# Kernel optimization log

Hardware: AMD Instinct MI355X
Metric: run time of the kernel (lower is better)

## Reference

```python
import jax, jax.numpy as jnp
import numpy as np

N, R, IN_DIM, OUT_DIM, MODE = 16, 128, 64, 64, 16


def setup_inputs() -> dict:
    key = jax.random.key(0)
    k1, k2, k3, k4, k5 = jax.random.split(key, 5)
    # xavier_normal-like scale used by the torch init:
    # std = gain * sqrt(2/(fan_in+fan_out)) with gain = sqrt(in+out)/(in*out)
    fan = IN_DIM * OUT_DIM * MODE * MODE  # torch fans over last-dim slices; scale is tiny either way
    w_std = (1.0 / (IN_DIM * OUT_DIM)) * np.sqrt(IN_DIM + OUT_DIM)
    return {
        "X": jax.random.normal(k1, (N, R, R, IN_DIM), dtype=jnp.float32),
        "w_res": jax.random.normal(k2, (IN_DIM, OUT_DIM), dtype=jnp.float32) / np.sqrt(IN_DIM),
        "b_res": jax.random.normal(k3, (OUT_DIM,), dtype=jnp.float32) * 0.01,
        "fw0": jax.random.normal(k4, (IN_DIM, OUT_DIM, MODE, MODE, 2), dtype=jnp.float32) * w_std,
        "fw1": jax.random.normal(k5, (IN_DIM, OUT_DIM, MODE, MODE, 2), dtype=jnp.float32) * w_std,
    }


def reference(X, w_res, b_res, fw0, fw1):
    # X: [N, r, r, in_dim]
    n, r, _, _ = X.shape
    m = MODE
    res = X @ w_res + b_res                          # [N, r, r, out]
    Xp = jnp.transpose(X, (0, 3, 1, 2))              # [N, in, r, r]
    X_ft = jnp.fft.rfft2(Xp, s=(r, r), norm="ortho")  # [N, in, r, r//2+1] complex
    W0 = fw0[..., 0] + 1j * fw0[..., 1]              # [in, out, m, m] complex
    W1 = fw1[..., 0] + 1j * fw1[..., 1]
    top = jnp.einsum("nihw,iohw->nohw", X_ft[:, :, :m, :m], W0)
    bot = jnp.einsum("nihw,iohw->nohw", X_ft[:, :, -m:, :m], W1)
    Out_ft = jnp.zeros((n, OUT_DIM, r, r // 2 + 1), dtype=top.dtype)
    Out_ft = Out_ft.at[:, :, :m, :m].set(top)
    Out_ft = Out_ft.at[:, :, -m:, :m].set(bot)
    Y = jnp.fft.irfft2(Out_ft, s=(r, r), norm="ortho")  # [N, out, r, r]
    Y = jnp.transpose(Y, (0, 2, 3, 1))                   # [N, r, r, out]
    return jax.nn.silu(Y + res)
```

## Files before the change

### kernel.cpp

```cpp
#include <hip/hip_runtime.h>

#define NBATCH 16
#define RSZ 128
#define ICH 64
#define OCH 64
#define MODES 16
#define TMODES 32
#define PI2F 6.283185307179586f

typedef float f32x4 __attribute__((ext_vector_type(4)));
typedef short bf16x8 __attribute__((ext_vector_type(8)));
typedef unsigned short u16x8 __attribute__((ext_vector_type(8)));

static __device__ __forceinline__ ushort f2bf(float f) {
  union { float f; unsigned u; } v;
  v.f = f;
  unsigned r = v.u + 0x7FFFu + ((v.u >> 16) & 1u);
  return (ushort)(r >> 16);
}
static __device__ __forceinline__ float b2f(ushort u) {
  union { unsigned u; float f; } v;
  v.u = ((unsigned)u) << 16;
  return v.f;
}
static __device__ __forceinline__ float2 twid(int p) {
  float a = PI2F * (float)p * (1.0f / 128.0f);
  return make_float2(__cosf(a), __sinf(a));
}

#define TAB_EF 4096
#define TAB_WR 8192
#define TAB_T1 12288
#define TAB_E2 28672

#define PREP_BLOCKS 138
#define DFTX_BLOCKS 2048

__global__ __launch_bounds__(256) void k_main(const float* __restrict__ X,
                                              const float* __restrict__ fw0,
                                              const float* __restrict__ fw1,
                                              const float* __restrict__ w_res,
                                              ushort2* __restrict__ A2,
                                              ushort* __restrict__ fwT,
                                              ushort* __restrict__ tabs) {
  const int tid = threadIdx.x;
  if (blockIdx.x < PREP_BLOCKS) {
    const int b = blockIdx.x;
    if (b < 128) {
      const int tensor = b >> 6, i = b & 63;
      const float* fw = tensor ? fw1 : fw0;
      const int o = tid & 63, q = tid >> 6;
      const float* src = fw + ((size_t)(i * 64 + o) * 256 + q * 64) * 2;
      ushort2* dst = (ushort2*)fwT;
#pragma unroll 4
      for (int r2 = 0; r2 < 32; ++r2) {
        float4 v = *(const float4*)(src + r2 * 4);
        int r = r2 * 2;
        int mh0 = q * 4 + (r >> 4), w0 = r & 15;
        int mh1 = q * 4 + ((r + 1) >> 4), w1 = (r + 1) & 15;
        int t0 = tensor * 16 + mh0, t1 = tensor * 16 + mh1;
        ushort2 p0, p1;
        p0.x = f2bf(v.x); p0.y = f2bf(v.y);
        p1.x = f2bf(v.z); p1.y = f2bf(v.w);
        dst[(((size_t)w0 * 32 + t0) * 64 + i) * 64 + o] = p0;
        dst[(((size_t)w1 * 32 + t1) * 64 + i) * 64 + o] = p1;
      }
      return;
    }
    __shared__ float2 utp[128];
    if (tid < 128) utp[tid] = twid(tid);
    __syncthreads();
    const int pb = b - 128;
    if (pb == 0) {
      for (int e = tid; e < 4096; e += 256) {
        int x = e >> 5, mm = e & 31, w = mm >> 1, c = mm & 1;
        float2 u = utp[(w * x) & 127];
        tabs[TAB_EF + e] = f2bf(c ? -u.y : u.x);
      }
    } else if (pb == 1) {
      for (int e = tid; e < 4096; e += 256) {
        int o = e >> 6, i = e & 63;
        tabs[TAB_WR + e] = f2bf(w_res[i * 64 + o]);
      }
    } else if (pb < 6) {
      for (int k = tid; k < 4096; k += 256) {
        int e = (pb - 2) * 4096 + k;
        int m = e >> 8, kk = e & 255;
        int y = kk & 127, pl = kk >> 7;
        int t = m & 31, imr = m >> 5;
        int h = (t < 16) ? t : (t + 96);
        float2 u = utp[(h * y) & 127];
        float val = (!imr) ? (pl ? u.y : u.x) : (pl ? u.x : -u.y);
        tabs[TAB_T1 + e] = f2bf(val);
      }
    } else {
      for (int k = tid; k < 4096; k += 256) {
        int e = (pb - 6) * 4096 + k;
        int m = e >> 6, kk = e & 63;
        int y = m & 127, imr = m >> 7;
        int t = kk & 31, pl = kk >> 5;
        int h = (t < 16) ? t : (t + 96);
        float2 u = utp[(h * y) & 127];
        float val = (!imr) ? (pl ? -u.y : u.x) : (pl ? u.x : u.y);
        tabs[TAB_E2 + e] = f2bf(val);
      }
    }
    return;
  }
  __shared__ float2 ut[128];
  __shared__ ushort Tm[32][136];
  __shared__ ushort XT[64][136];
  const int row = blockIdx.x - PREP_BLOCKS;
  const float* Xr = X + (size_t)row * RSZ * ICH;
  float4 rv[8];
#pragma unroll
  for (int e = 0; e < 2; ++e) {
    int r = tid + e * 256;
    int i0 = (r & 15) * 4, x0 = (r >> 4) * 4;
    rv[e * 4 + 0] = *(const float4*)&Xr[(x0 + 0) * ICH + i0];
    rv[e * 4 + 1] = *(const float4*)&Xr[(x0 + 1) * ICH + i0];
    rv[e * 4 + 2] = *(const float4*)&Xr[(x0 + 2) * ICH + i0];
    rv[e * 4 + 3] = *(const float4*)&Xr[(x0 + 3) * ICH + i0];
  }
  if (tid < 128) ut[tid] = twid(tid);
  __syncthreads();
#pragma unroll
  for (int e = 0; e < 16; ++e) {
    int idx = tid + e * 256;
    int m = idx >> 7, x = idx & 127;
    int w = m >> 1, c = m & 1;
    float2 u = ut[(w * x) & 127];
    Tm[m][x] = f2bf(c ? -u.y : u.x);
  }
#pragma unroll
  for (int e = 0; e < 2; ++e) {
    int r = tid + e * 256;
    int i0 = (r & 15) * 4, x0 = (r >> 4) * 4;
#pragma unroll
    for (int p = 0; p < 4; ++p) {
      int i = i0 + p;
      int col = x0 ^ ((((i) >> 2) & 7) << 3);
      ushort4 pk;
      pk.x = f2bf(((const float*)&rv[e * 4 + 0])[p]);
      pk.y = f2bf(((const float*)&rv[e * 4 + 1])[p]);
      pk.z = f2bf(((const float*)&rv[e * 4 + 2])[p]);
      pk.w = f2bf(((const float*)&rv[e * 4 + 3])[p]);
      *(ushort4*)&XT[i][col] = pk;
    }
  }
  __syncthreads();
  const int wid = tid >> 6, lane = tid & 63;
  const int lr = lane & 15, lk = lane >> 4;
  f32x4 acc[2];
  acc[0] = (f32x4)(0.f);
  acc[1] = (f32x4)(0.f);
#pragma unroll
  for (int kt = 0; kt < 4; ++kt) {
    int kb = kt * 32 + lk * 8;
    bf16x8 a0 = *(const bf16x8*)&Tm[lr][kb];
    bf16x8 a1 = *(const bf16x8*)&Tm[16 + lr][kb];
    int i = wid * 16 + lr;
    int col = kb ^ (((i >> 2) & 7) << 3);
    bf16x8 b = *(const bf16x8*)&XT[i][col];
    acc[0] = __builtin_amdgcn_mfma_f32_16x16x32_bf16(a0, b, acc[0], 0, 0, 0);
    acc[1] = __builtin_amdgcn_mfma_f32_16x16x32_bf16(a1, b, acc[1], 0, 0, 0);
  }
  {
    const int i = wid * 16 + lr;
#pragma unroll
    for (int mt = 0; mt < 2; ++mt) {
      int wb = mt * 8 + lk * 2;
      ushort2 p0, p1;
      p0.x = f2bf(acc[mt][0]); p0.y = f2bf(acc[mt][1]);
      p1.x = f2bf(acc[mt][2]); p1.y = f2bf(acc[mt][3]);
      A2[((size_t)row * MODES + wb) * ICH + i] = p0;
      A2[((size_t)row * MODES + wb + 1) * ICH + i] = p1;
    }
  }
}

__global__ __launch_bounds__(512) void k_mid(const ushort2* __restrict__ A2,
                                             const ushort* __restrict__ tabs,
                                             const ushort* __restrict__ fwT,
                                             ushort* __restrict__ D) {
  const int n = blockIdx.x >> 4;
  const int w = blockIdx.x & 15;
  __shared__ ushort As[64][264];
  __shared__ float2 Bls[32][66];
  __shared__ ushort Cs[64][72];
  const int tid = threadIdx.x;
  {
    const int i0 = (tid & 15) * 4, y0 = (tid >> 4) * 4;
    u16x8 vy[4];
#pragma unroll
    for (int dy = 0; dy < 4; ++dy)
      vy[dy] = *(const u16x8*)&A2[((size_t)(n * RSZ + y0 + dy) * MODES + w) * ICH + i0];
#pragma unroll
    for (int p = 0; p < 4; ++p) {
      ushort4 re, im;
      re.x = vy[0][2 * p];     re.y = vy[1][2 * p];     re.z = vy[2][2 * p];     re.w = vy[3][2 * p];
      im.x = vy[0][2 * p + 1]; im.y = vy[1][2 * p + 1]; im.z = vy[2][2 * p + 1]; im.w = vy[3][2 * p + 1];
      *(ushort4*)&As[i0 + p][y0] = re;
      *(ushort4*)&As[i0 + p][128 + y0] = im;
    }
  }
  __syncthreads();
  const int wid = tid >> 6, lane = tid & 63;
  const int lr = lane & 15, lk = lane >> 4;
  {
    const int mt = wid >> 1, nh = wid & 1;
    f32x4 acc[2];
    acc[0] = (f32x4)(0.f);
    acc[1] = (f32x4)(0.f);
#pragma unroll
    for (int kt = 0; kt < 8; ++kt) {
      int kb = kt * 32 + lk * 8;
      bf16x8 a = *(const bf16x8*)&tabs[TAB_T1 + (mt * 16 + lr) * 256 + kb];
      bf16x8 b0 = *(const bf16x8*)&As[(nh * 2 + 0) * 16 + lr][kb];
      bf16x8 b1 = *(const bf16x8*)&As[(nh * 2 + 1) * 16 + lr][kb];
      acc[0] = __builtin_amdgcn_mfma_f32_16x16x32_bf16(a, b0, acc[0], 0, 0, 0);
      acc[1] = __builtin_amdgcn_mfma_f32_16x16x32_bf16(a, b1, acc[1], 0, 0, 0);
    }
#pragma unroll
    for (int nt2 = 0; nt2 < 2; ++nt2)
#pragma unroll
      for (int q = 0; q < 4; ++q) {
        int m = mt * 16 + lk * 4 + q;
        int t = m & 31, pl = m >> 5;
        int i = (nh * 2 + nt2) * 16 + lr;
        ((float*)&Bls[t][i])[pl] = acc[nt2][q];
      }
  }
  __syncthreads();
  const float sc = (w == 0) ? (1.f / 16384.f) : (2.f / 16384.f);
  float2 cacc[4];
  const ushort2* fwT2 = (const ushort2*)fwT;
#pragma unroll
  for (int p = 0; p < 4; ++p) {
    const int t = p * 8 + wid;
    const ushort2* Wcol = fwT2 + (size_t)(w * 32 + t) * 4096 + lane;
    float cr = 0.f, ci = 0.f;
#pragma unroll 8
    for (int i = 0; i < 64; ++i) {
      ushort2 wv = Wcol[i * 64];
      float wr = b2f(wv.x), wi = b2f(wv.y);
      float2 b = Bls[t][i];
      cr += b.x * wr - b.y * wi;
      ci += b.x * wi + b.y * wr;
    }
    cacc[p] = make_float2(cr * sc, ci * sc);
  }
  __syncthreads();
#pragma unroll
  for (int p = 0; p < 4; ++p) {
    const int t = p * 8 + wid;
    Cs[lane][t] = f2bf(cacc[p].x);
    Cs[lane][t + 32] = f2bf(cacc[p].y);
  }
  __syncthreads();
  f32x4 acc[2][4];
#pragma unroll
  for (int mi = 0; mi < 2; ++mi)
#pragma unroll
    for (int nt = 0; nt < 4; ++nt) acc[mi][nt] = (f32x4)(0.f);
#pragma unroll
  for (int kt = 0; kt < 2; ++kt) {
    int kb = kt * 32 + lk * 8;
    bf16x8 b[4];
#pragma unroll
    for (int nt = 0; nt < 4; ++nt) b[nt] = *(const bf16x8*)&Cs[nt * 16 + lr][kb];
#pragma unroll
    for (int mi = 0; mi < 2; ++mi) {
      bf16x8 a = *(const bf16x8*)&tabs[TAB_E2 + ((wid * 2 + mi) * 16 + lr) * 64 + kb];
#pragma unroll
      for (int nt = 0; nt < 4; ++nt)
        acc[mi][nt] = __builtin_amdgcn_mfma_f32_16x16x32_bf16(a, b[nt], acc[mi][nt], 0, 0, 0);
    }
  }
#pragma unroll
  for (int mi = 0; mi < 2; ++mi)
#pragma unroll
    for (int nt = 0; nt < 4; ++nt)
#pragma unroll
      for (int q = 0; q < 4; ++q) {
        int m = (wid * 2 + mi) * 16 + lk * 4 + q;
        int y = m & 127, pl = m >> 7;
        int o = nt * 16 + lr;
        D[((size_t)(n * RSZ + y) * MODES + w) * 128 + o * 2 + pl] = f2bf(acc[mi][nt][q]);
      }
}

__global__ __launch_bounds__(256) void k_final(const float* __restrict__ X,
                                               const ushort* __restrict__ D,
                                               const ushort* __restrict__ tabs,
                                               const float* __restrict__ b_res,
                                               float* __restrict__ out) {
  __shared__ ushort Ac[128][104];
  __shared__ ushort Bc[64][104];
  __shared__ float br[64];
  const int tid = threadIdx.x;
  const int row = blockIdx.x;
  const float* Xr = X + (size_t)row * RSZ * ICH;
#pragma unroll
  for (int j = 0; j < 8; ++j) {
    int k = tid + j * 256;
    int x = k >> 4, i0 = (k & 15) * 4;
    float4 v = *(const float4*)&Xr[x * ICH + i0];
    ushort4 pk;
    pk.x = f2bf(v.x); pk.y = f2bf(v.y); pk.z = f2bf(v.z); pk.w = f2bf(v.w);
    *(ushort4*)&Ac[x][i0] = pk;
  }
  {
    int x = tid >> 1, half = tid & 1;
    *(bf16x8*)&Ac[x][64 + half * 16] = *(const bf16x8*)&tabs[TAB_EF + x * 32 + half * 16];
    *(bf16x8*)&Ac[x][64 + half * 16 + 8] = *(const bf16x8*)&tabs[TAB_EF + x * 32 + half * 16 + 8];
  }
  {
    int o = tid >> 2, s = (tid & 3) * 16;
    *(bf16x8*)&Bc[o][s] = *(const bf16x8*)&tabs[TAB_WR + o * 64 + s];
    *(bf16x8*)&Bc[o][s + 8] = *(const bf16x8*)&tabs[TAB_WR + o * 64 + s + 8];
  }
#pragma unroll
  for (int j = 0; j < 4; ++j) {
    int idx = tid + j * 256;
    int w2 = idx >> 6, o = idx & 63;
    ushort2 v = *(const ushort2*)&D[(size_t)row * 2048 + w2 * 128 + o * 2];
    *(ushort2*)&Bc[o][64 + 2 * w2] = v;
  }
  if (tid < 64) br[tid] = b_res[tid];
  __syncthreads();
  const int wid = tid >> 6, lane = tid & 63;
  const int lr = lane & 15, lk = lane >> 4;
  f32x4 acc[2][4];
#pragma unroll
  for (int mi = 0; mi < 2; ++mi)
#pragma unroll
    for (int nt = 0; nt < 4; ++nt) acc[mi][nt] = (f32x4)(0.f);
#pragma unroll
  for (int kt = 0; kt < 3; ++kt) {
    int kb = kt * 32 + lk * 8;
    bf16x8 a0 = *(const bf16x8*)&Ac[(wid * 2 + 0) * 16 + lr][kb];
    bf16x8 a1 = *(const bf16x8*)&Ac[(wid * 2 + 1) * 16 + lr][kb];
    bf16x8 b[4];
#pragma unroll
    for (int nt = 0; nt < 4; ++nt) b[nt] = *(const bf16x8*)&Bc[nt * 16 + lr][kb];
#pragma unroll
    for (int nt = 0; nt < 4; ++nt) {
      acc[0][nt] = __builtin_amdgcn_mfma_f32_16x16x32_bf16(a0, b[nt], acc[0][nt], 0, 0, 0);
      acc[1][nt] = __builtin_amdgcn_mfma_f32_16x16x32_bf16(a1, b[nt], acc[1][nt], 0, 0, 0);
    }
  }
  float* orow = out + (size_t)row * RSZ * OCH;
#pragma unroll
  for (int mi = 0; mi < 2; ++mi)
#pragma unroll
    for (int nt = 0; nt < 4; ++nt)
#pragma unroll
      for (int q = 0; q < 4; ++q) {
        int x = (wid * 2 + mi) * 16 + lk * 4 + q;
        int o = nt * 16 + lr;
        float v = acc[mi][nt][q] + br[o];
        orow[x * OCH + o] = v / (1.f + __expf(-v));
      }
}

extern "C" void kernel_launch(void* const* d_in, const int* in_sizes, int n_in,
                              void* d_out, int out_size, void* d_ws, size_t ws_size,
                              hipStream_t stream) {
  (void)in_sizes; (void)n_in; (void)out_size; (void)ws_size;
  const float* X = (const float*)d_in[0];
  const float* w_res = (const float*)d_in[1];
  const float* b_res = (const float*)d_in[2];
  const float* fw0 = (const float*)d_in[3];
  const float* fw1 = (const float*)d_in[4];
  float* out = (float*)d_out;
  ushort* wsu = (ushort*)d_ws;
  ushort2* A2 = (ushort2*)wsu;
  ushort* Dbf = wsu + 4194304;
  ushort* fwT = Dbf + 4194304;
  ushort* tabs = fwT + 4194304;
  k_main<<<PREP_BLOCKS + DFTX_BLOCKS, 256, 0, stream>>>(X, fw0, fw1, w_res, A2, fwT, tabs);
  k_mid<<<NBATCH * MODES, 512, 0, stream>>>(A2, tabs, fwT, Dbf);
  k_final<<<NBATCH * RSZ, 256, 0, stream>>>(X, Dbf, tabs, b_res, out);
}
```

Baseline: 64.92 us.

## Compute residual projection in k_main and pass bf16 result to k_final

Moves the X@w_res residual GEMM into k_main, reusing the X tile already loaded and converted to bf16 there, and stores the result as bf16 in workspace. k_final then starts its accumulators from this residual and only runs the spectral K-chunk, so it no longer reads X in fp32 or the w_res table. This adds a bf16 residual write/read round trip, extra LDS in k_main, and rounds the residual to bf16 before the final add.

After: 67.42 us. 3.8% more time.

```diff
diff --git a/kernel.cpp b/kernel.cpp
--- a/kernel.cpp
+++ b/kernel.cpp
@@ -29,11 +29,10 @@
 }
 
 #define TAB_EF 4096
-#define TAB_WR 8192
 #define TAB_T1 12288
 #define TAB_E2 28672
 
-#define PREP_BLOCKS 138
+#define PREP_BLOCKS 137
 #define DFTX_BLOCKS 2048
 
 __global__ __launch_bounds__(256) void k_main(const float* __restrict__ X,
@@ -42,6 +41,7 @@
                                               const float* __restrict__ w_res,
                                               ushort2* __restrict__ A2,
                                               ushort* __restrict__ fwT,
+                                              ushort* __restrict__ resb,
                                               ushort* __restrict__ tabs) {
   const int tid = threadIdx.x;
   if (blockIdx.x < PREP_BLOCKS) {
@@ -77,14 +77,9 @@
         float2 u = utp[(w * x) & 127];
         tabs[TAB_EF + e] = f2bf(c ? -u.y : u.x);
       }
-    } else if (pb == 1) {
-      for (int e = tid; e < 4096; e += 256) {
-        int o = e >> 6, i = e & 63;
-        tabs[TAB_WR + e] = f2bf(w_res[i * 64 + o]);
-      }
-    } else if (pb < 6) {
+    } else if (pb < 5) {
       for (int k = tid; k < 4096; k += 256) {
-        int e = (pb - 2) * 4096 + k;
+        int e = (pb - 1) * 4096 + k;
         int m = e >> 8, kk = e & 255;
         int y = kk & 127, pl = kk >> 7;
         int t = m & 31, imr = m >> 5;
@@ -95,7 +90,7 @@
       }
     } else {
       for (int k = tid; k < 4096; k += 256) {
-        int e = (pb - 6) * 4096 + k;
+        int e = (pb - 5) * 4096 + k;
         int m = e >> 6, kk = e & 63;
         int y = m & 127, imr = m >> 7;
         int t = kk & 31, pl = kk >> 5;
@@ -110,6 +105,8 @@
   __shared__ float2 ut[128];
   __shared__ ushort Tm[32][136];
   __shared__ ushort XT[64][136];
+  __shared__ ushort Xrm[128][76];
+  __shared__ ushort wrTs[64][76];
   const int row = blockIdx.x - PREP_BLOCKS;
   const float* Xr = X + (size_t)row * RSZ * ICH;
   float4 rv[8];
@@ -122,6 +119,18 @@
     rv[e * 4 + 2] = *(const float4*)&Xr[(x0 + 2) * ICH + i0];
     rv[e * 4 + 3] = *(const float4*)&Xr[(x0 + 3) * ICH + i0];
   }
+  {
+    int i = tid >> 2, oq = (tid & 3) * 16;
+    float4 wv0 = *(const float4*)&w_res[i * 64 + oq + 0];
+    float4 wv1 = *(const float4*)&w_res[i * 64 + oq + 4];
+    float4 wv2 = *(const float4*)&w_res[i * 64 + oq + 8];
+    float4 wv3 = *(const float4*)&w_res[i * 64 + oq + 12];
+    const float* wr4[4] = {(const float*)&wv0, (const float*)&wv1, (const float*)&wv2, (const float*)&wv3};
+#pragma unroll
+    for (int k = 0; k < 4; ++k)
+#pragma unroll
+      for (int c = 0; c < 4; ++c) wrTs[oq + k * 4 + c][i] = f2bf(wr4[k][c]);
+  }
   if (tid < 128) ut[tid] = twid(tid);
   __syncthreads();
 #pragma unroll
@@ -136,16 +145,26 @@
   for (int e = 0; e < 2; ++e) {
     int r = tid + e * 256;
     int i0 = (r & 15) * 4, x0 = (r >> 4) * 4;
+    ushort cc[4][4];
+#pragma unroll
+    for (int xr = 0; xr < 4; ++xr) {
+      const float* rp = (const float*)&rv[e * 4 + xr];
+#pragma unroll
+      for (int p = 0; p < 4; ++p) cc[xr][p] = f2bf(rp[p]);
+    }
 #pragma unroll
     for (int p = 0; p < 4; ++p) {
       int i = i0 + p;
       int col = x0 ^ ((((i) >> 2) & 7) << 3);
       ushort4 pk;
-      pk.x = f2bf(((const float*)&rv[e * 4 + 0])[p]);
-      pk.y = f2bf(((const float*)&rv[e * 4 + 1])[p]);
-      pk.z = f2bf(((const float*)&rv[e * 4 + 2])[p]);
-      pk.w = f2bf(((const float*)&rv[e * 4 + 3])[p]);
+      pk.x = cc[0][p]; pk.y = cc[1][p]; pk.z = cc[2][p]; pk.w = cc[3][p];
       *(ushort4*)&XT[i][col] = pk;
+    }
+#pragma unroll
+    for (int xr = 0; xr < 4; ++xr) {
+      ushort4 pk;
+      pk.x = cc[xr][0]; pk.y = cc[xr][1]; pk.z = cc[xr][2]; pk.w = cc[xr][3];
+      *(ushort4*)&Xrm[x0 + xr][i0] = pk;
     }
   }
   __syncthreads();
@@ -175,6 +194,40 @@
       p1.x = f2bf(acc[mt][2]); p1.y = f2bf(acc[mt][3]);
       A2[((size_t)row * MODES + wb) * ICH + i] = p0;
       A2[((size_t)row * MODES + wb + 1) * ICH + i] = p1;
+    }
+  }
+  f32x4 acc2[2][4];
+#pragma unroll
+  for (int mi = 0; mi < 2; ++mi)
+#pragma unroll
+    for (int nt = 0; nt < 4; ++nt) acc2[mi][nt] = (f32x4)(0.f);
+#pragma unroll
+  for (int kt2 = 0; kt2 < 2; ++kt2) {
+    int kb = kt2 * 32 + lk * 8;
+    bf16x8 a[2];
+#pragma unroll
+    for (int mi = 0; mi < 2; ++mi) a[mi] = *(const bf16x8*)&Xrm[(wid * 2 + mi) * 16 + lr][kb];
+#pragma unroll
+    for (int nt = 0; nt < 4; ++nt) {
+      bf16x8 b = *(const bf16x8*)&wrTs[nt * 16 + lr][kb];
+#pragma unroll
+      for (int mi = 0; mi < 2; ++mi)
+        acc2[mi][nt] = __builtin_amdgcn_mfma_f32_16x16x32_bf16(a[mi], b, acc2[mi][nt], 0, 0, 0);
+    }
+  }
+  {
+    ushort* rp = resb + (size_t)row * 8192 + tid * 32;
+#pragma unroll
+    for (int mi = 0; mi < 2; ++mi) {
+      ushort4 c0, c1, c2, c3;
+      c0.x = f2bf(acc2[mi][0][0]); c0.y = f2bf(acc2[mi][0][1]); c0.z = f2bf(acc2[mi][0][2]); c0.w = f2bf(acc2[mi][0][3]);
+      c1.x = f2bf(acc2[mi][1][0]); c1.y = f2bf(acc2[mi][1][1]); c1.z = f2bf(acc2[mi][1][2]); c1.w = f2bf(acc2[mi][1][3]);
+      c2.x = f2bf(acc2[mi][2][0]); c2.y = f2bf(acc2[mi][2][1]); c2.z = f2bf(acc2[mi][2][2]); c2.w = f2bf(acc2[mi][2][3]);
+      c3.x = f2bf(acc2[mi][3][0]); c3.y = f2bf(acc2[mi][3][1]); c3.z = f2bf(acc2[mi][3][2]); c3.w = f2bf(acc2[mi][3][3]);
+      *(ushort4*)&rp[mi * 16 + 0] = c0;
+      *(ushort4*)&rp[mi * 16 + 4] = c1;
+      *(ushort4*)&rp[mi * 16 + 8] = c2;
+      *(ushort4*)&rp[mi * 16 + 12] = c3;
     }
   }
 }
@@ -290,44 +343,35 @@
       }
 }
 
-__global__ __launch_bounds__(256) void k_final(const float* __restrict__ X,
+__global__ __launch_bounds__(256) void k_final(const ushort* __restrict__ resb,
                                                const ushort* __restrict__ D,
                                                const ushort* __restrict__ tabs,
                                                const float* __restrict__ b_res,
                                                float* __restrict__ out) {
-  __shared__ ushort Ac[128][104];
-  __shared__ ushort Bc[64][104];
+  __shared__ ushort Ac[128][40];
+  __shared__ ushort Bc[64][40];
   __shared__ float br[64];
   const int tid = threadIdx.x;
   const int row = blockIdx.x;
-  const float* Xr = X + (size_t)row * RSZ * ICH;
-#pragma unroll
-  for (int j = 0; j < 8; ++j) {
-    int k = tid + j * 256;
-    int x = k >> 4, i0 = (k & 15) * 4;
-    float4 v = *(const float4*)&Xr[x * ICH + i0];
-    ushort4 pk;
-    pk.x = f2bf(v.x); pk.y = f2bf(v.y); pk.z = f2bf(v.z); pk.w = f2bf(v.w);
-    *(ushort4*)&Ac[x][i0] = pk;
-  }
   {
     int x = tid >> 1, half = tid & 1;
-    *(bf16x8*)&Ac[x][64 + half * 16] = *(const bf16x8*)&tabs[TAB_EF + x * 32 + half * 16];
-    *(bf16x8*)&Ac[x][64 + half * 16 + 8] = *(const bf16x8*)&tabs[TAB_EF + x * 32 + half * 16 + 8];
-  }
-  {
-    int o = tid >> 2, s = (tid & 3) * 16;
-    *(bf16x8*)&Bc[o][s] = *(const bf16x8*)&tabs[TAB_WR + o * 64 + s];
-    *(bf16x8*)&Bc[o][s + 8] = *(const bf16x8*)&tabs[TAB_WR + o * 64 + s + 8];
+    *(bf16x8*)&Ac[x][half * 16] = *(const bf16x8*)&tabs[TAB_EF + x * 32 + half * 16];
+    *(bf16x8*)&Ac[x][half * 16 + 8] = *(const bf16x8*)&tabs[TAB_EF + x * 32 + half * 16 + 8];
   }
 #pragma unroll
   for (int j = 0; j < 4; ++j) {
     int idx = tid + j * 256;
     int w2 = idx >> 6, o = idx & 63;
     ushort2 v = *(const ushort2*)&D[(size_t)row * 2048 + w2 * 128 + o * 2];
-    *(ushort2*)&Bc[o][64 + 2 * w2] = v;
+    *(ushort2*)&Bc[o][2 * w2] = v;
   }
   if (tid < 64) br[tid] = b_res[tid];
+  const ushort* rp = resb + (size_t)row * 8192 + tid * 32;
+  u16x8 rch[4];
+  rch[0] = *(const u16x8*)&rp[0];
+  rch[1] = *(const u16x8*)&rp[8];
+  rch[2] = *(const u16x8*)&rp[16];
+  rch[3] = *(const u16x8*)&rp[24];
   __syncthreads();
   const int wid = tid >> 6, lane = tid & 63;
   const int lr = lane & 15, lk = lane >> 4;
@@ -335,10 +379,12 @@
 #pragma unroll
   for (int mi = 0; mi < 2; ++mi)
 #pragma unroll
-    for (int nt = 0; nt < 4; ++nt) acc[mi][nt] = (f32x4)(0.f);
-#pragma unroll
-  for (int kt = 0; kt < 3; ++kt) {
-    int kb = kt * 32 + lk * 8;
+    for (int nt = 0; nt < 4; ++nt)
+#pragma unroll
+      for (int q = 0; q < 4; ++q)
+        acc[mi][nt][q] = b2f((ushort)rch[mi * 2 + (nt >> 1)][(nt & 1) * 4 + q]);
+  {
+    int kb = lk * 8;
     bf16x8 a0 = *(const bf16x8*)&Ac[(wid * 2 + 0) * 16 + lr][kb];
     bf16x8 a1 = *(const bf16x8*)&Ac[(wid * 2 + 1) * 16 + lr][kb];
     bf16x8 b[4];
@@ -378,8 +424,9 @@
   ushort2* A2 = (ushort2*)wsu;
   ushort* Dbf = wsu + 4194304;
   ushort* fwT = Dbf + 4194304;
-  ushort* tabs = fwT + 4194304;
-  k_main<<<PREP_BLOCKS + DFTX_BLOCKS, 256, 0, stream>>>(X, fw0, fw1, w_res, A2, fwT, tabs);
+  ushort* resb = fwT + 4194304;
+  ushort* tabs = resb + 16777216;
+  k_main<<<PREP_BLOCKS + DFTX_BLOCKS, 256, 0, stream>>>(X, fw0, fw1, w_res, A2, fwT, resb, tabs);
   k_mid<<<NBATCH * MODES, 512, 0, stream>>>(A2, tabs, fwT, Dbf);
-  k_final<<<NBATCH * RSZ, 256, 0, stream>>>(X, Dbf, tabs, b_res, out);
-}
+  k_final<<<NBATCH * RSZ, 256, 0, stream>>>(resb, Dbf, tabs, b_res, out);
+}
```

## Process four X rows per block with double-buffered LDS and register prefetch

Applied to the files above, without the earlier changes.

The DFT-along-x stage now gives each block four rows instead of one, so the grid shrinks from 2048 to 512 DFT blocks. Each block builds the twiddle matrix Tm once and reuses it across its rows. It also prefetches the next row's X into registers while the current row is converted and multiplied, using two LDS buffers so loads overlap compute. The cost is fewer blocks, which lowers parallelism and latency hiding, plus higher register and LDS use per block.

After: 65.48 us. No clear change (+0.9%).

```diff
diff --git a/kernel.cpp b/kernel.cpp
--- a/kernel.cpp
+++ b/kernel.cpp
@@ -34,7 +34,71 @@
 #define TAB_E2 28672
 
 #define PREP_BLOCKS 138
-#define DFTX_BLOCKS 2048
+#define DFTX_BLOCKS 512
+
+static __device__ __forceinline__ void load_row(float4 rv[8], const float* __restrict__ X,
+                                                 int row, int tid) {
+  const float* Xr = X + (size_t)row * RSZ * ICH;
+#pragma unroll
+  for (int e = 0; e < 2; ++e) {
+    int r = tid + e * 256;
+    int i0 = (r & 15) * 4, x0 = (r >> 4) * 4;
+    rv[e * 4 + 0] = *(const float4*)&Xr[(x0 + 0) * ICH + i0];
+    rv[e * 4 + 1] = *(const float4*)&Xr[(x0 + 1) * ICH + i0];
+    rv[e * 4 + 2] = *(const float4*)&Xr[(x0 + 2) * ICH + i0];
+    rv[e * 4 + 3] = *(const float4*)&Xr[(x0 + 3) * ICH + i0];
+  }
+}
+
+static __device__ __forceinline__ void conv_row(const float4 rv[8], ushort (*XTb)[136], int tid) {
+#pragma unroll
+  for (int e = 0; e < 2; ++e) {
+    int r = tid + e * 256;
+    int i0 = (r & 15) * 4, x0 = (r >> 4) * 4;
+#pragma unroll
+    for (int p = 0; p < 4; ++p) {
+      int i = i0 + p;
+      int col = x0 ^ ((((i) >> 2) & 7) << 3);
+      ushort4 pk;
+      pk.x = f2bf(((const float*)&rv[e * 4 + 0])[p]);
+      pk.y = f2bf(((const float*)&rv[e * 4 + 1])[p]);
+      pk.z = f2bf(((const float*)&rv[e * 4 + 2])[p]);
+      pk.w = f2bf(((const float*)&rv[e * 4 + 3])[p]);
+      *(ushort4*)&XTb[i][col] = pk;
+    }
+  }
+}
+
+static __device__ __forceinline__ void mfma_row(const ushort (*XTb)[136],
+                                                const ushort (*Tm)[136],
+                                                ushort2* __restrict__ A2, int row, int tid) {
+  const int wid = tid >> 6, lane = tid & 63;
+  const int lr = lane & 15, lk = lane >> 4;
+  f32x4 acc[2];
+  acc[0] = (f32x4)(0.f);
+  acc[1] = (f32x4)(0.f);
+#pragma unroll
+  for (int kt = 0; kt < 4; ++kt) {
+    int kb = kt * 32 + lk * 8;
+    bf16x8 a0 = *(const bf16x8*)&Tm[lr][kb];
+    bf16x8 a1 = *(const bf16x8*)&Tm[16 + lr][kb];
+    int i = wid * 16 + lr;
+    int col = kb ^ (((i >> 2) & 7) << 3);
+    bf16x8 b = *(const bf16x8*)&XTb[i][col];
+    acc[0] = __builtin_amdgcn_mfma_f32_16x16x32_bf16(a0, b, acc[0], 0, 0, 0);
+    acc[1] = __builtin_amdgcn_mfma_f32_16x16x32_bf16(a1, b, acc[1], 0, 0, 0);
+  }
+  const int i = wid * 16 + lr;
+#pragma unroll
+  for (int mt = 0; mt < 2; ++mt) {
+    int wb = mt * 8 + lk * 2;
+    ushort2 p0, p1;
+    p0.x = f2bf(acc[mt][0]); p0.y = f2bf(acc[mt][1]);
+    p1.x = f2bf(acc[mt][2]); p1.y = f2bf(acc[mt][3]);
+    A2[((size_t)row * MODES + wb) * ICH + i] = p0;
+    A2[((size_t)row * MODES + wb + 1) * ICH + i] = p1;
+  }
+}
 
 __global__ __launch_bounds__(256) void k_main(const float* __restrict__ X,
                                               const float* __restrict__ fw0,
@@ -109,19 +173,10 @@
   }
   __shared__ float2 ut[128];
   __shared__ ushort Tm[32][136];
-  __shared__ ushort XT[64][136];
-  const int row = blockIdx.x - PREP_BLOCKS;
-  const float* Xr = X + (size_t)row * RSZ * ICH;
-  float4 rv[8];
-#pragma unroll
-  for (int e = 0; e < 2; ++e) {
-    int r = tid + e * 256;
-    int i0 = (r & 15) * 4, x0 = (r >> 4) * 4;
-    rv[e * 4 + 0] = *(const float4*)&Xr[(x0 + 0) * ICH + i0];
-    rv[e * 4 + 1] = *(const float4*)&Xr[(x0 + 1) * ICH + i0];
-    rv[e * 4 + 2] = *(const float4*)&Xr[(x0 + 2) * ICH + i0];
-    rv[e * 4 + 3] = *(const float4*)&Xr[(x0 + 3) * ICH + i0];
-  }
+  __shared__ ushort XT[2][64][136];
+  const int row0 = (blockIdx.x - PREP_BLOCKS) * 4;
+  float4 rvA[8], rvB[8];
+  load_row(rvA, X, row0 + 0, tid);
   if (tid < 128) ut[tid] = twid(tid);
   __syncthreads();
 #pragma unroll
@@ -132,51 +187,21 @@
     float2 u = ut[(w * x) & 127];
     Tm[m][x] = f2bf(c ? -u.y : u.x);
   }
-#pragma unroll
-  for (int e = 0; e < 2; ++e) {
-    int r = tid + e * 256;
-    int i0 = (r & 15) * 4, x0 = (r >> 4) * 4;
-#pragma unroll
-    for (int p = 0; p < 4; ++p) {
-      int i = i0 + p;
-      int col = x0 ^ ((((i) >> 2) & 7) << 3);
-      ushort4 pk;
-      pk.x = f2bf(((const float*)&rv[e * 4 + 0])[p]);
-      pk.y = f2bf(((const float*)&rv[e * 4 + 1])[p]);
-      pk.z = f2bf(((const float*)&rv[e * 4 + 2])[p]);
-      pk.w = f2bf(((const float*)&rv[e * 4 + 3])[p]);
-      *(ushort4*)&XT[i][col] = pk;
-    }
-  }
-  __syncthreads();
-  const int wid = tid >> 6, lane = tid & 63;
-  const int lr = lane & 15, lk = lane >> 4;
-  f32x4 acc[2];
-  acc[0] = (f32x4)(0.f);
-  acc[1] = (f32x4)(0.f);
-#pragma unroll
-  for (int kt = 0; kt < 4; ++kt) {
-    int kb = kt * 32 + lk * 8;
-    bf16x8 a0 = *(const bf16x8*)&Tm[lr][kb];
-    bf16x8 a1 = *(const bf16x8*)&Tm[16 + lr][kb];
-    int i = wid * 16 + lr;
-    int col = kb ^ (((i >> 2) & 7) << 3);
-    bf16x8 b = *(const bf16x8*)&XT[i][col];
-    acc[0] = __builtin_amdgcn_mfma_f32_16x16x32_bf16(a0, b, acc[0], 0, 0, 0);
-    acc[1] = __builtin_amdgcn_mfma_f32_16x16x32_bf16(a1, b, acc[1], 0, 0, 0);
-  }
-  {
-    const int i = wid * 16 + lr;
-#pragma unroll
-    for (int mt = 0; mt < 2; ++mt) {
-      int wb = mt * 8 + lk * 2;
-      ushort2 p0, p1;
-      p0.x = f2bf(acc[mt][0]); p0.y = f2bf(acc[mt][1]);
-      p1.x = f2bf(acc[mt][2]); p1.y = f2bf(acc[mt][3]);
-      A2[((size_t)row * MODES + wb) * ICH + i] = p0;
-      A2[((size_t)row * MODES + wb + 1) * ICH + i] = p1;
-    }
-  }
+  conv_row(rvA, XT[0], tid);
+  load_row(rvB, X, row0 + 1, tid);
+  __syncthreads();
+  mfma_row(XT[0], Tm, A2, row0 + 0, tid);
+  conv_row(rvB, XT[1], tid);
+  load_row(rvA, X, row0 + 2, tid);
+  __syncthreads();
+  mfma_row(XT[1], Tm, A2, row0 + 1, tid);
+  conv_row(rvA, XT[0], tid);
+  load_row(rvB, X, row0 + 3, tid);
+  __syncthreads();
+  mfma_row(XT[0], Tm, A2, row0 + 2, tid);
+  conv_row(rvB, XT[1], tid);
+  __syncthreads();
+  mfma_row(XT[1], Tm, A2, row0 + 3, tid);
 }
 
 __global__ __launch_bounds__(512) void k_mid(const ushort2* __restrict__ A2,
```
